# Optimization experiments

Hardware: AMD Instinct MI355X
Metric: run time of the kernel (lower is better)

## Reference

```python
import jax, jax.numpy as jnp
import numpy as np

N_NODES = 100000
N_EDGES = 3200000
N_FEAT = 256
HIDDEN = 64
N_CLASSES = 6


def gcn_conv(x, W, b, src, dst, n_nodes):
    """PyG GCNConv: out = D^{-1/2} (A + I) D^{-1/2} X W + b (self-loops added)."""
    h = x @ W  # [N, out]
    loops = jnp.arange(n_nodes, dtype=src.dtype)
    src2 = jnp.concatenate([src, loops])
    dst2 = jnp.concatenate([dst, loops])
    # degree over destination nodes (edge weight 1), including self-loops
    deg = jax.ops.segment_sum(jnp.ones_like(dst2, dtype=h.dtype), dst2,
                              num_segments=n_nodes)
    dis = jnp.where(deg > 0, jax.lax.rsqrt(deg), 0.0)  # deg^{-1/2}
    norm = dis[src2] * dis[dst2]  # [E+N]
    msg = h[src2] * norm[:, None]  # gather + scale
    out = jax.ops.segment_sum(msg, dst2, num_segments=n_nodes)  # scatter-add
    return out + b


def setup_inputs() -> dict:
    key = jax.random.key(0)
    ks = jax.random.split(key, 5)
    x = jax.random.normal(ks[0], (N_NODES, N_FEAT), dtype=jnp.float32)
    edge_index = jax.random.randint(ks[1], (2, N_EDGES), 0, N_NODES, dtype=jnp.int64)
    W1 = jax.random.normal(ks[2], (N_FEAT, HIDDEN), dtype=jnp.float32) / np.sqrt(N_FEAT)
    b1 = jnp.zeros((HIDDEN,), dtype=jnp.float32)
    W2 = jax.random.normal(ks[3], (HIDDEN, HIDDEN), dtype=jnp.float32) / np.sqrt(HIDDEN)
    b2 = jnp.zeros((HIDDEN,), dtype=jnp.float32)
    Wfc = jax.random.normal(ks[4], (HIDDEN, N_CLASSES), dtype=jnp.float32) / np.sqrt(HIDDEN)
    bfc = jnp.zeros((N_CLASSES,), dtype=jnp.float32)
    return {"x": x, "edge_index": edge_index, "W1": W1, "b1": b1,
            "W2": W2, "b2": b2, "Wfc": Wfc, "bfc": bfc}


def reference(x, edge_index, W1, b1, W2, b2, Wfc, bfc):
    src, dst = edge_index[0], edge_index[1]
    n = x.shape[0]
    h = jax.nn.relu(gcn_conv(x, W1, b1, src, dst, n))
    # dropout(p=0.2) is identity in eval mode
    h = jax.nn.relu(gcn_conv(h, W2, b2, src, dst, n))
    return h @ Wfc + bfc
```

## Files before the change

kernel.cpp:

```cpp
#include <hip/hip_runtime.h>
#include <hip/hip_fp16.h>
#include <math.h>

#define NFEAT 256
#define HID 64
#define NCLS 6
#define NBMX 1600
#define CAPB 4096
#define CHUNK 16384
#define FUSED_LDS 32768

typedef float vf4 __attribute__((ext_vector_type(4)));
typedef int   vi4 __attribute__((ext_vector_type(4)));


__global__ __launch_bounds__(256) void k_count(const int* __restrict__ dst,
                                               int* __restrict__ C, int E, int nbuck) {
  __shared__ int cnt[NBMX];
  int t = threadIdx.x;
  for (int i = t; i < nbuck; i += 256) cnt[i] = 0;
  __syncthreads();
  int e0 = blockIdx.x * CHUNK;
  int e1 = e0 + CHUNK;
  if (e1 > E) e1 = E;
  for (int r0 = e0; r0 < e1; r0 += 1024) {
    int i0 = r0 + t * 4;
    if (i0 + 4 <= e1) {
      vi4 dv = __builtin_nontemporal_load((const vi4*)&dst[i0]);
      atomicAdd(&cnt[dv.x >> 6], 1);
      atomicAdd(&cnt[dv.y >> 6], 1);
      atomicAdd(&cnt[dv.z >> 6], 1);
      atomicAdd(&cnt[dv.w >> 6], 1);
    } else {
      for (int q = 0; q < 4; ++q)
        if (i0 + q < e1) atomicAdd(&cnt[dst[i0 + q] >> 6], 1);
    }
  }
  __syncthreads();
  int* Crow = C + (size_t)blockIdx.x * nbuck;
  for (int i = t; i < nbuck; i += 256) Crow[i] = cnt[i];
}


__global__ __launch_bounds__(256) void k_scan_cols(int* __restrict__ C,
                                                   int* __restrict__ T,
                                                   int nblk, int nbuck) {
  int b = blockIdx.x * 256 + threadIdx.x;
  if (b >= nbuck) return;
  int run = 0;
  int blk = 0;
  for (; blk + 4 <= nblk; blk += 4) {
    int c0 = C[(size_t)(blk + 0) * nbuck + b];
    int c1 = C[(size_t)(blk + 1) * nbuck + b];
    int c2 = C[(size_t)(blk + 2) * nbuck + b];
    int c3 = C[(size_t)(blk + 3) * nbuck + b];
    C[(size_t)(blk + 0) * nbuck + b] = run; run += c0;
    C[(size_t)(blk + 1) * nbuck + b] = run; run += c1;
    C[(size_t)(blk + 2) * nbuck + b] = run; run += c2;
    C[(size_t)(blk + 3) * nbuck + b] = run; run += c3;
  }
  for (; blk < nblk; ++blk) {
    int c = C[(size_t)blk * nbuck + b];
    C[(size_t)blk * nbuck + b] = run;
    run += c;
  }
  T[b] = run;
}


__global__ __launch_bounds__(256) void k_scanb(const int* __restrict__ T,
                                               int* __restrict__ bbase, int nbuck) {
  __shared__ int sh[256];
  __shared__ int carry;
  int t = threadIdx.x;
  if (t == 0) carry = 0;
  __syncthreads();
  for (int base = 0; base < nbuck; base += 256) {
    int v = (base + t < nbuck) ? T[base + t] : 0;
    sh[t] = v;
    __syncthreads();
    for (int off = 1; off < 256; off <<= 1) {
      int x = sh[t];
      int y = (t >= off) ? sh[t - off] : 0;
      __syncthreads();
      sh[t] = x + y;
      __syncthreads();
    }
    if (base + t < nbuck) bbase[base + t] = carry + sh[t] - v;
    __syncthreads();
    if (t == 255) carry += sh[255];
    __syncthreads();
  }
}


__global__ __launch_bounds__(256) void k_fused(const int* __restrict__ src,
                                               const int* __restrict__ dst,
                                               const int* __restrict__ C,
                                               const int* __restrict__ bbase,
                                               unsigned* __restrict__ packed,
                                               int E, int nbuck, int nbb,
                                               const float* __restrict__ X,
                                               const float* __restrict__ W1,
                                               __half* __restrict__ H16, int n) {
  extern __shared__ char smem[];
  int t = threadIdx.x;

  if (blockIdx.x < nbb) {
    int* baseL = (int*)smem;
    int* cnt   = baseL + NBMX;
    const int* Crow = C + (size_t)blockIdx.x * nbuck;
    for (int i = t; i < nbuck; i += 256) {
      baseL[i] = bbase[i] + Crow[i];
      cnt[i] = 0;
    }
    __syncthreads();

    int e0 = blockIdx.x * CHUNK;
    int e1 = e0 + CHUNK;
    if (e1 > E) e1 = E;
    for (int r0 = e0; r0 < e1; r0 += 1024) {
      int i0 = r0 + t * 4;
      int s4[4], d4[4];
      bool full = (i0 + 4 <= e1);
      if (full) {
        vi4 sv = __builtin_nontemporal_load((const vi4*)&src[i0]);
        vi4 dv = __builtin_nontemporal_load((const vi4*)&dst[i0]);
        s4[0] = sv.x; s4[1] = sv.y; s4[2] = sv.z; s4[3] = sv.w;
        d4[0] = dv.x; d4[1] = dv.y; d4[2] = dv.z; d4[3] = dv.w;
      } else {
        for (int q = 0; q < 4; ++q)
          if (i0 + q < e1) { s4[q] = src[i0 + q]; d4[q] = dst[i0 + q]; }
      }
#pragma unroll
      for (int q = 0; q < 4; ++q) {
        if (i0 + q < e1) {
          int b = d4[q] >> 6;
          int slot = atomicAdd(&cnt[b], 1);
          packed[(size_t)baseL[b] + slot] =
              ((unsigned)s4[q] << 6) | (unsigned)(d4[q] & 63);
        }
      }
    }
  } else {
    float* Wl = (float*)smem;
    float* Xl = Wl + 4096;
    const int row0 = (blockIdx.x - nbb) * 64;
    const int tc = t & 15;
    const int tr = t >> 4;
    float acc[4][4] = {};

    for (int k0 = 0; k0 < NFEAT; k0 += 64) {
      __syncthreads();
#pragma unroll
      for (int i = 0; i < 4; ++i) {
        int idx = t * 4 + i * 1024;
        int kr = idx >> 6, c = idx & 63;
        *(vf4*)&Wl[idx] = *(const vf4*)&W1[(size_t)(k0 + kr) * 64 + c];
      }
#pragma unroll
      for (int i = 0; i < 4; ++i) {
        int idx = t * 4 + i * 1024;
        int r = idx >> 6, c = idx & 63;
        int row = row0 + r;
        vf4 v = {0.f, 0.f, 0.f, 0.f};
        if (row < n) v = __builtin_nontemporal_load((const vf4*)&X[(size_t)row * NFEAT + k0 + c]);
        *(vf4*)&Xl[idx] = v;
      }
      __syncthreads();
#pragma unroll 4
      for (int kk = 0; kk < 64; kk += 4) {
        float4 xv[4], wv[4];
#pragma unroll
        for (int r = 0; r < 4; ++r) xv[r] = *(float4*)&Xl[(tr * 4 + r) * 64 + kk];
#pragma unroll
        for (int q = 0; q < 4; ++q) wv[q] = *(float4*)&Wl[(kk + q) * 64 + tc * 4];
#pragma unroll
        for (int r = 0; r < 4; ++r) {
          const float xr[4] = {xv[r].x, xv[r].y, xv[r].z, xv[r].w};
#pragma unroll
          for (int q = 0; q < 4; ++q) {
            acc[r][0] += xr[q] * wv[q].x;
            acc[r][1] += xr[q] * wv[q].y;
            acc[r][2] += xr[q] * wv[q].z;
            acc[r][3] += xr[q] * wv[q].w;
          }
        }
      }
    }
#pragma unroll
    for (int r = 0; r < 4; ++r) {
      int row = row0 + tr * 4 + r;
      if (row < n) {
        __half2 h01 = __floats2half2_rn(acc[r][0], acc[r][1]);
        __half2 h23 = __floats2half2_rn(acc[r][2], acc[r][3]);
        uint2 st;
        st.x = *reinterpret_cast<unsigned*>(&h01);
        st.y = *reinterpret_cast<unsigned*>(&h23);
        ((uint2*)H16)[(size_t)row * 16 + tc] = st;
      }
    }
  }
}


__global__ __launch_bounds__(256) void k_build(unsigned* __restrict__ packed,
                                               const int* __restrict__ T,
                                               const int* __restrict__ bbase,
                                               int2* __restrict__ rowrange,
                                               float* __restrict__ dis,
                                               int n, int nbuck) {
  __shared__ unsigned buf[CAPB];
  __shared__ unsigned outb[CAPB];
  __shared__ int cnt4[4][64];
  __shared__ int cur4[4][64];
  __shared__ int offi[64];
  __shared__ int offx[64];
  __shared__ int cntl[64];
  int b = blockIdx.x;
  int t = threadIdx.x;
  int g = t >> 6;
  int m = T[b];
  if (m > CAPB) m = CAPB;
  int bb = bbase[b];
  unsigned* pb = packed + bb;

  cnt4[g][t & 63] = 0;
  for (int k = t; k < m; k += 256) buf[k] = pb[k];
  __syncthreads();
  for (int k = t; k < m; k += 256) atomicAdd(&cnt4[g][buf[k] & 63u], 1);
  __syncthreads();
  if (t < 64) {
    int c0 = cnt4[0][t], c1 = cnt4[1][t], c2 = cnt4[2][t], c3 = cnt4[3][t];
    int tot = c0 + c1 + c2 + c3;
    cntl[t] = tot;
    offi[t] = tot;
    cur4[0][t] = 0;
    cur4[1][t] = c0;
    cur4[2][t] = c0 + c1;
    cur4[3][t] = c0 + c1 + c2;
  }
  __syncthreads();
  for (int off = 1; off < 64; off <<= 1) {
    int x = (t < 64) ? offi[t] : 0;
    int y = (t >= off && t < 64) ? offi[t - off] : 0;
    __syncthreads();
    if (t < 64) offi[t] = x + y;
    __syncthreads();
  }
  if (t < 64) {
    offx[t] = offi[t] - cntl[t];
    int v = b * 64 + t;
    if (v < n) {
      rowrange[v] = make_int2(bb + offx[t], cntl[t]);
      dis[v] = rsqrtf((float)cntl[t] + 1.0f);
    }
#pragma unroll
    for (int gg = 0; gg < 4; ++gg) cur4[gg][t] += offx[t];
  }
  __syncthreads();
  for (int k = t; k < m; k += 256) {
    unsigned e = buf[k];
    int dl = e & 63u;
    int q = atomicAdd(&cur4[g][dl], 1);
    outb[q] = e >> 6;
  }
  __syncthreads();
  for (int k = t; k < m; k += 256) pb[k] = outb[k];
}


__global__ __launch_bounds__(256) void k_agg_gemm(const int2* __restrict__ rowrange,
                                                  const int* __restrict__ srcs,
                                                  const __half* __restrict__ g16,
                                                  const float* __restrict__ dis,
                                                  const float* __restrict__ b1,
                                                  const float* __restrict__ W2,
                                                  __half* __restrict__ g2out, int n) {
  __shared__ float W2l[64 * 64];
  __shared__ float arow[16][68];
  int t = threadIdx.x;
  for (int i = t * 4; i < 4096; i += 1024)
    *(vf4*)&W2l[i] = *(const vf4*)&W2[i];

  int grp = t >> 4, lane = t & 15;
  int v = blockIdx.x * 16 + grp;
  bool active = (v < n);
  const uint2* g2 = (const uint2*)g16;

  float rx = 0.f, ry = 0.f, rz = 0.f, rw = 0.f;
  if (active) {
    int2 rr = rowrange[v];
    int j = rr.x, end = rr.x + rr.y;
    float dv = dis[v];
    uint2 su = g2[(size_t)v * 16 + lane];
    float2 f0 = __half22float2(*reinterpret_cast<__half2*>(&su.x));
    float2 f1 = __half22float2(*reinterpret_cast<__half2*>(&su.y));
    float ax = dv * f0.x, ay = dv * f0.y, az = dv * f1.x, aw = dv * f1.y;

    for (; j + 8 <= end; j += 8) {
      int s[8];
#pragma unroll
      for (int q = 0; q < 8; ++q) s[q] = __builtin_nontemporal_load(&srcs[j + q]);
      float ds[8];
      uint2 a[8];
#pragma unroll
      for (int q = 0; q < 8; ++q) { ds[q] = dis[s[q]]; a[q] = g2[(size_t)s[q] * 16 + lane]; }
#pragma unroll
      for (int q = 0; q < 8; ++q) {
        float2 p0 = __half22float2(*reinterpret_cast<__half2*>(&a[q].x));
        float2 p1 = __half22float2(*reinterpret_cast<__half2*>(&a[q].y));
        ax = fmaf(ds[q], p0.x, ax); ay = fmaf(ds[q], p0.y, ay);
        az = fmaf(ds[q], p1.x, az); aw = fmaf(ds[q], p1.y, aw);
      }
    }
    for (; j < end; ++j) {
      int s0 = __builtin_nontemporal_load(&srcs[j]);
      float ds = dis[s0];
      uint2 a0 = g2[(size_t)s0 * 16 + lane];
      float2 p0 = __half22float2(*reinterpret_cast<__half2*>(&a0.x));
      float2 p1 = __half22float2(*reinterpret_cast<__half2*>(&a0.y));
      ax = fmaf(ds, p0.x, ax); ay = fmaf(ds, p0.y, ay);
      az = fmaf(ds, p1.x, az); aw = fmaf(ds, p1.y, aw);
    }
    float4 bb = *(const float4*)&b1[lane * 4];
    rx = fmaxf(fmaf(dv, ax, bb.x), 0.f);
    ry = fmaxf(fmaf(dv, ay, bb.y), 0.f);
    rz = fmaxf(fmaf(dv, az, bb.z), 0.f);
    rw = fmaxf(fmaf(dv, aw, bb.w), 0.f);
  }
  arow[grp][lane * 4 + 0] = rx;
  arow[grp][lane * 4 + 1] = ry;
  arow[grp][lane * 4 + 2] = rz;
  arow[grp][lane * 4 + 3] = rw;
  __syncthreads();

  if (active) {
    float o0 = 0.f, o1 = 0.f, o2 = 0.f, o3 = 0.f;
    int c = lane * 4;
#pragma unroll 4
    for (int k = 0; k < 64; ++k) {
      float a = arow[grp][k];
      vf4 w = *(const vf4*)&W2l[k * 64 + c];
      o0 = fmaf(a, w.x, o0);
      o1 = fmaf(a, w.y, o1);
      o2 = fmaf(a, w.z, o2);
      o3 = fmaf(a, w.w, o3);
    }
    float dvv = dis[v];
    __half2 h01 = __floats2half2_rn(o0 * dvv, o1 * dvv);
    __half2 h23 = __floats2half2_rn(o2 * dvv, o3 * dvv);
    uint2 st;
    st.x = *reinterpret_cast<unsigned*>(&h01);
    st.y = *reinterpret_cast<unsigned*>(&h23);
    ((uint2*)g2out)[(size_t)v * 16 + lane] = st;
  }
}


__global__ __launch_bounds__(256) void k_agg_fc(const int2* __restrict__ rowrange,
                                                const int* __restrict__ srcs,
                                                const __half* __restrict__ g16,
                                                const float* __restrict__ dis,
                                                const float* __restrict__ b2,
                                                const float* __restrict__ Wfc,
                                                const float* __restrict__ bfc,
                                                float* __restrict__ outp, int n) {
  __shared__ float Wl[64 * NCLS];
  __shared__ float bl[8];
  int t = threadIdx.x;
  for (int i = t; i < 64 * NCLS; i += 256) Wl[i] = Wfc[i];
  if (t < NCLS) bl[t] = bfc[t];
  __syncthreads();

  int grp = t >> 4, lane = t & 15;
  int v = blockIdx.x * 16 + grp;
  bool active = (v < n);
  const uint2* g2 = (const uint2*)g16;

  float r0 = 0.f, r1 = 0.f, r2 = 0.f, r3 = 0.f;
  if (active) {
    int2 rr = rowrange[v];
    int j = rr.x, end = rr.x + rr.y;
    uint2 su = g2[(size_t)v * 16 + lane];
    float2 f0 = __half22float2(*reinterpret_cast<__half2*>(&su.x));
    float2 f1 = __half22float2(*reinterpret_cast<__half2*>(&su.y));
    float ax = f0.x, ay = f0.y, az = f1.x, aw = f1.y;

    for (; j + 8 <= end; j += 8) {
      int s[8];
#pragma unroll
      for (int q = 0; q < 8; ++q) s[q] = __builtin_nontemporal_load(&srcs[j + q]);
      uint2 a[8];
#pragma unroll
      for (int q = 0; q < 8; ++q) a[q] = g2[(size_t)s[q] * 16 + lane];
#pragma unroll
      for (int q = 0; q < 8; ++q) {
        float2 p0 = __half22float2(*reinterpret_cast<__half2*>(&a[q].x));
        float2 p1 = __half22float2(*reinterpret_cast<__half2*>(&a[q].y));
        ax += p0.x; ay += p0.y; az += p1.x; aw += p1.y;
      }
    }
    for (; j < end; ++j) {
      int s0 = __builtin_nontemporal_load(&srcs[j]);
      uint2 a0 = g2[(size_t)s0 * 16 + lane];
      float2 p0 = __half22float2(*reinterpret_cast<__half2*>(&a0.x));
      float2 p1 = __half22float2(*reinterpret_cast<__half2*>(&a0.y));
      ax += p0.x; ay += p0.y; az += p1.x; aw += p1.y;
    }
    float dv = dis[v];
    float4 bb = *(const float4*)&b2[lane * 4];
    r0 = fmaxf(fmaf(dv, ax, bb.x), 0.f);
    r1 = fmaxf(fmaf(dv, ay, bb.y), 0.f);
    r2 = fmaxf(fmaf(dv, az, bb.z), 0.f);
    r3 = fmaxf(fmaf(dv, aw, bb.w), 0.f);
  }

  float p[NCLS];
#pragma unroll
  for (int jj = 0; jj < NCLS; ++jj) p[jj] = 0.f;
  int k0 = lane * 4;
#pragma unroll
  for (int q = 0; q < 4; ++q) {
    float a = (q == 0) ? r0 : (q == 1) ? r1 : (q == 2) ? r2 : r3;
#pragma unroll
    for (int jj = 0; jj < NCLS; ++jj)
      p[jj] = fmaf(a, Wl[(k0 + q) * NCLS + jj], p[jj]);
  }
#pragma unroll
  for (int m = 1; m < 16; m <<= 1) {
#pragma unroll
    for (int jj = 0; jj < NCLS; ++jj)
      p[jj] += __shfl_xor(p[jj], m, 64);
  }
  if (active && lane < NCLS)
    outp[(size_t)v * NCLS + lane] = p[lane] + bl[lane];
}


extern "C" void kernel_launch(void* const* d_in, const int* in_sizes, int n_in,
                              void* d_out, int out_size, void* d_ws, size_t ws_size,
                              hipStream_t stream) {
  const float* x   = (const float*)d_in[0];
  const int*   ei  = (const int*)d_in[1];
  const float* W1  = (const float*)d_in[2];
  const float* b1  = (const float*)d_in[3];
  const float* W2  = (const float*)d_in[4];
  const float* b2  = (const float*)d_in[5];
  const float* Wfc = (const float*)d_in[6];
  const float* bfc = (const float*)d_in[7];
  float* out = (float*)d_out;

  const int n = in_sizes[0] / NFEAT;
  const int E = in_sizes[1] / 2;
  const int* src = ei;
  const int* dst = ei + E;
  const int nbuck = (n + 63) >> 6;
  const int nbb = (E + CHUNK - 1) / CHUNK;
  const int ntile = (n + 63) / 64;

  char* ws = (char*)d_ws;
  size_t off = 0;
  auto alloc = [&](size_t bytes) -> void* {
    void* p = (void*)(ws + off);
    off += (bytes + 255) & ~(size_t)255;
    return p;
  };
  float* dis      = (float*)alloc((size_t)n * 4);
  int2*  rowrange = (int2*)alloc((size_t)n * 8);
  int*   C        = (int*)alloc((size_t)nbb * nbuck * 4);
  int*   T        = (int*)alloc((size_t)nbuck * 4);
  int*   bbase    = (int*)alloc((size_t)nbuck * 4);
  unsigned* packed = (unsigned*)alloc((size_t)E * 4);
  __half* bufA16  = (__half*)alloc((size_t)n * HID * 2);
  __half* bufC16  = (__half*)alloc((size_t)n * HID * 2);

  k_count<<<nbb, 256, 0, stream>>>(dst, C, E, nbuck);
  k_scan_cols<<<(nbuck + 255) / 256, 256, 0, stream>>>(C, T, nbb, nbuck);
  k_scanb<<<1, 256, 0, stream>>>(T, bbase, nbuck);
  k_fused<<<nbb + ntile, 256, FUSED_LDS, stream>>>(src, dst, C, bbase, packed,
                                                   E, nbuck, nbb, x, W1, bufA16, n);
  k_build<<<nbuck, 256, 0, stream>>>(packed, T, bbase, rowrange, dis, n, nbuck);

  k_agg_gemm<<<(n + 15) / 16, 256, 0, stream>>>(rowrange, (const int*)packed, bufA16,
                                                dis, b1, W2, bufC16, n);

  k_agg_fc<<<(n + 15) / 16, 256, 0, stream>>>(rowrange, (const int*)packed, bufC16,
                                              dis, b2, Wfc, bfc, out, n);
}
```

Before: 286.2 us.

## Stage edge bucketing in LDS before contiguous writeback; unroll gathers by 16

The edge-scatter half of the fused kernel now sorts its chunk into buckets in LDS first. It computes per-bucket counts from the column-scanned count matrix, prefix-sums them in the block, and then copies each bucket out as one contiguous run. Before, every edge was scattered straight to global memory. CHUNK is halved so a chunk's entries fit in the enlarged LDS allocation. Both aggregation kernels get a 16-wide unrolled gather loop for more loads in flight, at the cost of more registers and lower occupancy.

```diff
diff --git a/kernel.cpp b/kernel.cpp
--- a/kernel.cpp
+++ b/kernel.cpp
@@ -7,8 +7,8 @@
 #define NCLS 6
 #define NBMX 1600
 #define CAPB 4096
-#define CHUNK 16384
-#define FUSED_LDS 32768
+#define CHUNK 8192
+#define FUSED_LDS 45568
 
 typedef float vf4 __attribute__((ext_vector_type(4)));
 typedef int   vi4 __attribute__((ext_vector_type(4)));
@@ -97,6 +97,7 @@
 __global__ __launch_bounds__(256) void k_fused(const int* __restrict__ src,
                                                const int* __restrict__ dst,
                                                const int* __restrict__ C,
+                                               const int* __restrict__ T,
                                                const int* __restrict__ bbase,
                                                unsigned* __restrict__ packed,
                                                int E, int nbuck, int nbb,
@@ -104,15 +105,44 @@
                                                const float* __restrict__ W1,
                                                __half* __restrict__ H16, int n) {
   extern __shared__ char smem[];
+  __shared__ int tsum[256];
   int t = threadIdx.x;
 
   if (blockIdx.x < nbb) {
-    int* baseL = (int*)smem;
-    int* cnt   = baseL + NBMX;
+    int* offs = (int*)smem;
+    int* cur  = offs + NBMX;
+    unsigned* entries = (unsigned*)(cur + NBMX);
     const int* Crow = C + (size_t)blockIdx.x * nbuck;
-    for (int i = t; i < nbuck; i += 256) {
-      baseL[i] = bbase[i] + Crow[i];
-      cnt[i] = 0;
+    bool last = (blockIdx.x == nbb - 1);
+    const int* CrowN = C + (size_t)(blockIdx.x + 1) * nbuck;
+
+    for (int b = t; b < nbuck; b += 256)
+      offs[b] = (last ? T[b] : CrowN[b]) - Crow[b];
+    __syncthreads();
+    int base0 = t * 7;
+    int c7[7];
+    int s = 0;
+#pragma unroll
+    for (int i = 0; i < 7; ++i) {
+      int b = base0 + i;
+      c7[i] = (b < nbuck) ? offs[b] : 0;
+      s += c7[i];
+    }
+    tsum[t] = s;
+    __syncthreads();
+    for (int off = 1; off < 256; off <<= 1) {
+      int x = tsum[t];
+      int y = (t >= off) ? tsum[t - off] : 0;
+      __syncthreads();
+      tsum[t] = x + y;
+      __syncthreads();
+    }
+    int run = tsum[t] - s;
+#pragma unroll
+    for (int i = 0; i < 7; ++i) {
+      int b = base0 + i;
+      if (b < nbuck) { offs[b] = run; cur[b] = run; }
+      run += c7[i];
     }
     __syncthreads();
 
@@ -136,10 +166,17 @@
       for (int q = 0; q < 4; ++q) {
         if (i0 + q < e1) {
           int b = d4[q] >> 6;
-          int slot = atomicAdd(&cnt[b], 1);
-          packed[(size_t)baseL[b] + slot] =
-              ((unsigned)s4[q] << 6) | (unsigned)(d4[q] & 63);
+          int p = atomicAdd(&cur[b], 1);
+          entries[p] = ((unsigned)s4[q] << 6) | (unsigned)(d4[q] & 63);
         }
+      }
+    }
+    __syncthreads();
+    for (int b = t; b < nbuck; b += 256) {
+      int lb = offs[b], le = cur[b];
+      if (le > lb) {
+        unsigned* g = &packed[(size_t)bbase[b] + Crow[b]];
+        for (int k = lb; k < le; ++k) g[k - lb] = entries[k];
       }
     }
   } else {
@@ -298,6 +335,22 @@
     float2 f1 = __half22float2(*reinterpret_cast<__half2*>(&su.y));
     float ax = dv * f0.x, ay = dv * f0.y, az = dv * f1.x, aw = dv * f1.y;
 
+    for (; j + 16 <= end; j += 16) {
+      int s[16];
+#pragma unroll
+      for (int q = 0; q < 16; ++q) s[q] = __builtin_nontemporal_load(&srcs[j + q]);
+      float ds[16];
+      uint2 a[16];
+#pragma unroll
+      for (int q = 0; q < 16; ++q) { ds[q] = dis[s[q]]; a[q] = g2[(size_t)s[q] * 16 + lane]; }
+#pragma unroll
+      for (int q = 0; q < 16; ++q) {
+        float2 p0 = __half22float2(*reinterpret_cast<__half2*>(&a[q].x));
+        float2 p1 = __half22float2(*reinterpret_cast<__half2*>(&a[q].y));
+        ax = fmaf(ds[q], p0.x, ax); ay = fmaf(ds[q], p0.y, ay);
+        az = fmaf(ds[q], p1.x, az); aw = fmaf(ds[q], p1.y, aw);
+      }
+    }
     for (; j + 8 <= end; j += 8) {
       int s[8];
 #pragma unroll
@@ -387,6 +440,20 @@
     float2 f1 = __half22float2(*reinterpret_cast<__half2*>(&su.y));
     float ax = f0.x, ay = f0.y, az = f1.x, aw = f1.y;
 
+    for (; j + 16 <= end; j += 16) {
+      int s[16];
+#pragma unroll
+      for (int q = 0; q < 16; ++q) s[q] = __builtin_nontemporal_load(&srcs[j + q]);
+      uint2 a[16];
+#pragma unroll
+      for (int q = 0; q < 16; ++q) a[q] = g2[(size_t)s[q] * 16 + lane];
+#pragma unroll
+      for (int q = 0; q < 16; ++q) {
+        float2 p0 = __half22float2(*reinterpret_cast<__half2*>(&a[q].x));
+        float2 p1 = __half22float2(*reinterpret_cast<__half2*>(&a[q].y));
+        ax += p0.x; ay += p0.y; az += p1.x; aw += p1.y;
+      }
+    }
     for (; j + 8 <= end; j += 8) {
       int s[8];
 #pragma unroll
@@ -478,7 +545,7 @@
   k_count<<<nbb, 256, 0, stream>>>(dst, C, E, nbuck);
   k_scan_cols<<<(nbuck + 255) / 256, 256, 0, stream>>>(C, T, nbb, nbuck);
   k_scanb<<<1, 256, 0, stream>>>(T, bbase, nbuck);
-  k_fused<<<nbb + ntile, 256, FUSED_LDS, stream>>>(src, dst, C, bbase, packed,
+  k_fused<<<nbb + ntile, 256, FUSED_LDS, stream>>>(src, dst, C, T, bbase, packed,
                                                    E, nbuck, nbb, x, W1, bufA16, n);
   k_build<<<nbuck, 256, 0, stream>>>(packed, T, bbase, rowrange, dis, n, nbuck);
 
```

Result: slower. 313.3 us (+9.5%).
